# Kernel tuning notes

Measured on AMD Instinct MI355X. Metric: run time of the kernel, lower is better.

## Reference

```python
import jax, jax.numpy as jnp
import numpy as np

EMB_DIM = 1024
ATT_DIM = 1024

def setup_inputs() -> dict:
    key = jax.random.key(0)
    ks = jax.random.split(key, 7)
    B, S = 8, 2048
    x_h = jax.random.normal(ks[0], (B, S, EMB_DIM), dtype=jnp.float32)
    # Linear params (stored as [in, out] for x @ W + b)
    sq = 1.0 / np.sqrt(EMB_DIM)
    Wq = jax.random.uniform(ks[1], (EMB_DIM, ATT_DIM), jnp.float32, -sq, sq)
    bq = jax.random.uniform(ks[2], (ATT_DIM,), jnp.float32, -sq, sq)
    Wk = jax.random.uniform(ks[3], (EMB_DIM, ATT_DIM), jnp.float32, -sq, sq)
    bk = jax.random.uniform(ks[4], (ATT_DIM,), jnp.float32, -sq, sq)
    Wv = jax.random.uniform(ks[5], (EMB_DIM, EMB_DIM), jnp.float32, -sq, sq)
    bv = jax.random.uniform(ks[6], (EMB_DIM,), jnp.float32, -sq, sq)
    return {"x_h": x_h, "Wq": Wq, "bq": bq, "Wk": Wk, "bk": bk, "Wv": Wv, "bv": bv}

def reference(x_h, Wq, bq, Wk, bk, Wv, bv):
    q = x_h @ Wq + bq               # [B,S,att_dim]
    k = x_h @ Wk + bk               # [B,S,att_dim]
    v = x_h @ Wv + bv               # [B,S,emb_dim]
    scale = 1.0 / jnp.sqrt(jnp.asarray(k.shape[-1], q.dtype))
    scores = jnp.einsum('bqd,bkd->bqk', q, k) * scale   # [B,S,S]
    # NOTE: original softmaxes over dim=1 (the QUERY axis), not the key axis.
    attn = jax.nn.softmax(scores, axis=1)
    return jnp.einsum('bqk,bkd->bqd', attn, v)
```

## Files before the change

### kernel.cpp

```cpp
#include <hip/hip_runtime.h>
#include <math.h>

typedef __bf16 bf16x8 __attribute__((ext_vector_type(8)));
typedef float f32x4 __attribute__((ext_vector_type(4)));
typedef unsigned short ushort8 __attribute__((ext_vector_type(8)));
typedef unsigned short ushort4v __attribute__((ext_vector_type(4)));
typedef unsigned short u16;

#define DEVINL __device__ __forceinline__

DEVINL u16 f2bf(float f) {
    union { float f; unsigned u; } a; a.f = f;
    unsigned u = a.u;
    return (u16)((u + 0x7FFFu + ((u >> 16) & 1u)) >> 16);
}
DEVINL float bf2f(u16 h) { return __uint_as_float(((unsigned)h) << 16); }

DEVINL void gload_lds16(const void* g, void* l) {
    __builtin_amdgcn_global_load_lds(
        (__attribute__((address_space(1))) void*)(g),
        (__attribute__((address_space(3))) void*)(l),
        16, 0, 0);
}

template<int EPI>
__global__ __launch_bounds__(512, 2)
void gemm256(const u16* __restrict__ A, int lda, long sAz,
             const u16* __restrict__ B, int ldb, long sBz,
             void* __restrict__ Cv, int ldc, long sCz,
             const float* __restrict__ bias, float* __restrict__ part,
             float scale, int K)
{
    __shared__ u16 lds[65536];
    const int tid = threadIdx.x;
    const int tile_x = blockIdx.x, tile_y = blockIdx.y;
    const long bz = blockIdx.z;

    const u16* Ab = A + bz * sAz;
    const u16* Bb = B + bz * sBz;
    const int row0 = tile_x * 256, col0 = tile_y * 256;

    const int sr = tid >> 2;
    const int csw = ((tid & 3) * 16) ^ (((sr >> 1) & 3) << 4);
    const u16* Ag = Ab + (long)(row0 + sr) * lda + (csw >> 1);
    const u16* Bg = Bb + (long)(col0 + sr) * ldb + (csw >> 1);
    const int dst0 = tid * 8;

    const int lane = tid & 63, wid = tid >> 6;
    const int wm = wid >> 2, wn = wid & 3;
    const int lane_r = lane & 15;
    const int rdcol = (((lane >> 4) * 16) ^ (((lane_r >> 1) & 3) << 4)) >> 1;
    const int arow0 = wm * 128 + lane_r;
    const int brow0 = wn * 64 + lane_r;

    const int NT = K >> 6;
    f32x4 acc[8][4] = {};
    bf16x8 aF0[4], bF0[4], aF1[4], bF1[4];

    auto issueA = [&](int t1, int s, int b) {
        const u16* g = Ag + (long)t1 * 64 + s * 32;
        u16* d = &lds[(b * 2 + s) * 8192 + dst0];
        gload_lds16(g, d);
        gload_lds16(g + (long)128 * lda, d + 4096);
    };
    auto issueB = [&](int t1, int s, int b) {
        const u16* g = Bg + (long)t1 * 64 + s * 32;
        u16* d = &lds[32768 + (b * 2 + s) * 8192 + dst0];
        gload_lds16(g, d);
        gload_lds16(g + (long)128 * ldb, d + 4096);
    };

#define READ_AB(bufv, s, h, SET)                                            \
    _Pragma("unroll")                                                       \
    for (int m = 0; m < 4; ++m)                                             \
        aF##SET[m] = *(const bf16x8*)&lds[((bufv) * 2 + (s)) * 8192 +       \
                         (arow0 + (h) * 64 + m * 16) * 32 + rdcol];         \
    _Pragma("unroll")                                                       \
    for (int n = 0; n < 4; ++n)                                             \
        bF##SET[n] = *(const bf16x8*)&lds[32768 + ((bufv) * 2 + (s)) * 8192 \
                         + (brow0 + n * 16) * 32 + rdcol];

#define MFMA16S(SET, h)                                                     \
    __builtin_amdgcn_s_setprio(1);                                          \
    _Pragma("unroll")                                                       \
    for (int m = 0; m < 4; ++m)                                             \
        _Pragma("unroll")                                                   \
        for (int n = 0; n < 4; ++n)                                         \
            acc[(h) * 4 + m][n] = __builtin_amdgcn_mfma_f32_16x16x32_bf16(  \
                bF##SET[n], aF##SET[m], acc[(h) * 4 + m][n], 0, 0, 0);      \
    __builtin_amdgcn_s_setprio(0);

#define GATE(n)                                                             \
    asm volatile("s_waitcnt vmcnt(" #n ")" ::: "memory");                   \
    __builtin_amdgcn_s_barrier();

    issueA(0, 0, 0); issueB(0, 0, 0);
    issueA(0, 1, 0); issueB(0, 1, 0);
    GATE(4);
    READ_AB(0, 0, 0, 0);

    for (int t = 0; t < NT - 1; ++t) {
        const int buf = t & 1, nbuf = buf ^ 1;
        issueA(t + 1, 0, nbuf); issueB(t + 1, 0, nbuf);
        READ_AB(buf, 0, 1, 1);
        MFMA16S(0, 0);
        GATE(4);
        READ_AB(buf, 1, 0, 0);
        MFMA16S(1, 1);
        issueA(t + 1, 1, nbuf); issueB(t + 1, 1, nbuf);
        READ_AB(buf, 1, 1, 1);
        MFMA16S(0, 0);
        GATE(4);
        READ_AB(nbuf, 0, 0, 0);
        MFMA16S(1, 1);
    }
    {
        const int buf = (NT - 1) & 1;
        READ_AB(buf, 0, 1, 1);
        MFMA16S(0, 0);
        GATE(0);
        READ_AB(buf, 1, 0, 0);
        MFMA16S(1, 1);
        READ_AB(buf, 1, 1, 1);
        MFMA16S(0, 0);
        MFMA16S(1, 1);
    }
#undef READ_AB
#undef MFMA16S
#undef GATE

    const int erow = lane & 15, ecol0 = (lane >> 4) * 4;
    float4 bias4[4];
    if constexpr (EPI == 0) {
#pragma unroll
        for (int nf = 0; nf < 4; ++nf)
            bias4[nf] = *(const float4*)&bias[col0 + wn * 64 + nf * 16 + ecol0];
    }
    f32x4 csum[4] = {};
#pragma unroll
    for (int mf = 0; mf < 8; ++mf) {
        const int gr = row0 + wm * 128 + mf * 16 + erow;
#pragma unroll
        for (int nf = 0; nf < 4; ++nf) {
            const int gc = col0 + wn * 64 + nf * 16 + ecol0;
            f32x4 v = acc[mf][nf];
            if constexpr (EPI == 0) {
                v[0] += bias4[nf].x; v[1] += bias4[nf].y;
                v[2] += bias4[nf].z; v[3] += bias4[nf].w;
                ushort4v o = { f2bf(v[0]), f2bf(v[1]), f2bf(v[2]), f2bf(v[3]) };
                *(ushort4v*)((u16*)Cv + bz * sCz + (long)gr * ldc + gc) = o;
            } else if constexpr (EPI == 1) {
                f32x4 e;
#pragma unroll
                for (int r = 0; r < 4; ++r) e[r] = __expf(v[r] * scale);
                csum[nf] += e;
                ushort4v o = { f2bf(e[0]), f2bf(e[1]), f2bf(e[2]), f2bf(e[3]) };
                *(ushort4v*)((u16*)Cv + bz * sCz + (long)gr * ldc + gc) = o;
            } else {
                *(float4*)((float*)Cv + bz * sCz + (long)gr * ldc + gc) =
                    make_float4(v[0], v[1], v[2], v[3]);
            }
        }
    }
    if constexpr (EPI == 1) {
#pragma unroll
        for (int nf = 0; nf < 4; ++nf)
#pragma unroll
            for (int r = 0; r < 4; ++r) {
                float s = csum[nf][r];
                s += __shfl_xor(s, 1);
                s += __shfl_xor(s, 2);
                s += __shfl_xor(s, 4);
                s += __shfl_xor(s, 8);
                csum[nf][r] = s;
            }
        if ((lane & 15) == 0) {
#pragma unroll
            for (int nf = 0; nf < 4; ++nf) {
                float* p = part + ((bz * 16 + (long)tile_x * 2 + wm) * 2048)
                         + col0 + wn * 64 + nf * 16 + ecol0;
                *(float4*)p = make_float4(csum[nf][0], csum[nf][1],
                                          csum[nf][2], csum[nf][3]);
            }
        }
    }
}

__global__ void cast_x_k(const float* __restrict__ x, u16* __restrict__ o)
{
    const int i = blockIdx.x * 256 + threadIdx.x;
    const float4* xv = (const float4*)x;
    const float4 a = xv[(long)i * 2], b = xv[(long)i * 2 + 1];
    ushort8 r;
    r[0] = f2bf(a.x); r[1] = f2bf(a.y); r[2] = f2bf(a.z); r[3] = f2bf(a.w);
    r[4] = f2bf(b.x); r[5] = f2bf(b.y); r[6] = f2bf(b.z); r[7] = f2bf(b.w);
    *(ushort8*)(o + (long)i * 8) = r;
}

__global__ void wt_k(const float* __restrict__ Wq, const float* __restrict__ Wk,
                     const float* __restrict__ Wv, u16* __restrict__ Wt)
{
    __shared__ float t[32][33];
    const int z = blockIdx.z;
    const float* W = (z == 0) ? Wq : ((z == 1) ? Wk : Wv);
    const int k0 = blockIdx.x * 32, n0 = blockIdx.y * 32;
    const int tx = threadIdx.x, ty = threadIdx.y;
#pragma unroll
    for (int j = 0; j < 32; j += 8)
        t[ty + j][tx] = W[(long)(k0 + ty + j) * 1024 + n0 + tx];
    __syncthreads();
#pragma unroll
    for (int j = 0; j < 32; j += 8)
        Wt[((long)z * 1024 + n0 + ty + j) * 1024 + k0 + tx] = f2bf(t[tx][ty + j]);
}

__global__ void bias_k(const float* __restrict__ bq, const float* __restrict__ bk,
                       const float* __restrict__ bv, float* __restrict__ bcat)
{
    const int i = blockIdx.x * 256 + threadIdx.x;
    bcat[i] = (i < 1024) ? bq[i] : ((i < 2048) ? bk[i - 1024] : bv[i - 2048]);
}

__global__ void rcp_k(const float* __restrict__ part, float* __restrict__ rden)
{
    const int b = blockIdx.y;
    const int k = blockIdx.x * 256 + threadIdx.x;
    float s = 0.f;
#pragma unroll
    for (int c = 0; c < 16; ++c) s += part[((long)b * 16 + c) * 2048 + k];
    rden[b * 2048 + k] = 1.0f / s;
}

__global__ void vt_k(const u16* __restrict__ qkv, const float* __restrict__ rden,
                     u16* __restrict__ Vt)
{
    __shared__ float t[32][33];
    const int b = blockIdx.z;
    const int k0 = blockIdx.x * 32, d0 = blockIdx.y * 32;
    const int tx = threadIdx.x, ty = threadIdx.y;
#pragma unroll
    for (int j = 0; j < 32; j += 8) {
        const int k = k0 + ty + j;
        t[ty + j][tx] = bf2f(qkv[((long)b * 2048 + k) * 3072 + 2048 + d0 + tx])
                        * rden[b * 2048 + k];
    }
    __syncthreads();
#pragma unroll
    for (int j = 0; j < 32; j += 8)
        Vt[((long)b * 1024 + d0 + ty + j) * 2048 + k0 + tx] = f2bf(t[tx][ty + j]);
}

extern "C" void kernel_launch(void* const* d_in, const int* in_sizes, int n_in,
                              void* d_out, int out_size, void* d_ws, size_t ws_size,
                              hipStream_t stream)
{
    const float* x  = (const float*)d_in[0];
    const float* Wq = (const float*)d_in[1];
    const float* bq = (const float*)d_in[2];
    const float* Wk = (const float*)d_in[3];
    const float* bk = (const float*)d_in[4];
    const float* Wv = (const float*)d_in[5];
    const float* bv = (const float*)d_in[6];

    char* ws = (char*)d_ws;
    u16*   qkv  = (u16*)(ws);
    u16*   E    = (u16*)(ws + 100663296);
    u16*   Vt   = (u16*)(ws + 167772160);
    u16*   xb   = (u16*)(ws + 201326592);
    u16*   Wt   = (u16*)(ws + 234881024);
    float* bcat = (float*)(ws + 241172480);
    float* part = (float*)(ws + 241184768);
    float* rden = (float*)(ws + 243281920);

    const long sQKV = (long)2048 * 3072;
    const long sE   = (long)2048 * 2048;
    const long sVt  = (long)1024 * 2048;
    const long sO   = (long)2048 * 1024;

    cast_x_k<<<8192, 256, 0, stream>>>(x, xb);
    wt_k<<<dim3(32, 32, 3), dim3(32, 8), 0, stream>>>(Wq, Wk, Wv, Wt);
    bias_k<<<12, 256, 0, stream>>>(bq, bk, bv, bcat);
    gemm256<0><<<dim3(64, 12, 1), 512, 0, stream>>>(
        xb, 1024, 0, Wt, 1024, 0, qkv, 3072, 0, bcat, nullptr, 0.f, 1024);
    gemm256<1><<<dim3(8, 8, 8), 512, 0, stream>>>(
        qkv, 3072, sQKV, qkv + 1024, 3072, sQKV, E, 2048, sE,
        nullptr, part, 0.03125f, 1024);
    rcp_k<<<dim3(8, 8), 256, 0, stream>>>(part, rden);
    vt_k<<<dim3(64, 32, 8), dim3(32, 8), 0, stream>>>(qkv, rden, Vt);
    gemm256<2><<<dim3(8, 4, 8), 512, 0, stream>>>(
        E, 2048, sE, Vt, 2048, sVt, d_out, 1024, sO,
        nullptr, nullptr, 1.f, 2048);
}
```

Baseline: 301.0 us.

## Switch GEMM inner loop to 32x32x16 MFMA with barrier-fenced ping-pong schedule

Replaces the 16x16x32 bf16 MFMA tiling with 32x32x16 MFMA, so each wave holds a 4x2 grid of 32x32 accumulators and reads fewer, larger fragments from LDS. The main loop is restructured into eight-MFMA phases fenced by s_barrier, interleaving LDS reads and global-to-LDS issues between them. The epilogue is rewritten for the 32x32 output layout, including a wider shuffle reduction for column sums. The goal is to cut LDS read traffic per FLOP and improve MFMA issue density, at the cost of many extra barriers that may serialize waves.

```diff
diff --git a/kernel.cpp b/kernel.cpp
--- a/kernel.cpp
+++ b/kernel.cpp
@@ -3,6 +3,7 @@
 
 typedef __bf16 bf16x8 __attribute__((ext_vector_type(8)));
 typedef float f32x4 __attribute__((ext_vector_type(4)));
+typedef float f32x16 __attribute__((ext_vector_type(16)));
 typedef unsigned short ushort8 __attribute__((ext_vector_type(8)));
 typedef unsigned short ushort4v __attribute__((ext_vector_type(4)));
 typedef unsigned short u16;
@@ -48,14 +49,14 @@
 
     const int lane = tid & 63, wid = tid >> 6;
     const int wm = wid >> 2, wn = wid & 3;
-    const int lane_r = lane & 15;
-    const int rdcol = (((lane >> 4) * 16) ^ (((lane_r >> 1) & 3) << 4)) >> 1;
-    const int arow0 = wm * 128 + lane_r;
-    const int brow0 = wn * 64 + lane_r;
+    const int l31 = lane & 31, eh = lane >> 5;
+    const int eh16 = eh * 16;
+    const int am0 = wm * 128 + l31;
+    const int bn0 = wn * 64 + l31;
 
     const int NT = K >> 6;
-    f32x4 acc[8][4] = {};
-    bf16x8 aF0[4], bF0[4], aF1[4], bF1[4];
+    f32x16 acc[4][2] = {};
+    bf16x8 afr[2][2], bfr[2][2];
 
     auto issueA = [&](int t1, int s, int b) {
         const u16* g = Ag + (long)t1 * 64 + s * 32;
@@ -70,24 +71,37 @@
         gload_lds16(g + (long)128 * ldb, d + 4096);
     };
 
-#define READ_AB(bufv, s, h, SET)                                            \
+#define RDIDX(r, ks) \
+    ((((r) * 64 + ((((ks) * 32) + eh16) ^ ((((r) >> 1) & 3) << 4))) >> 1))
+
+#define READ_A32(bufv, s, h)                                                \
     _Pragma("unroll")                                                       \
-    for (int m = 0; m < 4; ++m)                                             \
-        aF##SET[m] = *(const bf16x8*)&lds[((bufv) * 2 + (s)) * 8192 +       \
-                         (arow0 + (h) * 64 + m * 16) * 32 + rdcol];         \
+    for (int m2 = 0; m2 < 2; ++m2)                                          \
+        _Pragma("unroll")                                                   \
+        for (int ks = 0; ks < 2; ++ks)                                      \
+            afr[m2][ks] = *(const bf16x8*)&lds[((bufv) * 2 + (s)) * 8192    \
+                + RDIDX(am0 + ((h) * 2 + m2) * 32, ks)];
+
+#define READ_B32(bufv, s)                                                   \
     _Pragma("unroll")                                                       \
-    for (int n = 0; n < 4; ++n)                                             \
-        bF##SET[n] = *(const bf16x8*)&lds[32768 + ((bufv) * 2 + (s)) * 8192 \
-                         + (brow0 + n * 16) * 32 + rdcol];
-
-#define MFMA16S(SET, h)                                                     \
+    for (int nf = 0; nf < 2; ++nf)                                          \
+        _Pragma("unroll")                                                   \
+        for (int ks = 0; ks < 2; ++ks)                                      \
+            bfr[nf][ks] = *(const bf16x8*)&lds[32768 +                      \
+                ((bufv) * 2 + (s)) * 8192 + RDIDX(bn0 + nf * 32, ks)];
+
+#define MFMA8(h)                                                            \
     __builtin_amdgcn_s_setprio(1);                                          \
     _Pragma("unroll")                                                       \
-    for (int m = 0; m < 4; ++m)                                             \
+    for (int m2 = 0; m2 < 2; ++m2)                                          \
         _Pragma("unroll")                                                   \
-        for (int n = 0; n < 4; ++n)                                         \
-            acc[(h) * 4 + m][n] = __builtin_amdgcn_mfma_f32_16x16x32_bf16(  \
-                bF##SET[n], aF##SET[m], acc[(h) * 4 + m][n], 0, 0, 0);      \
+        for (int nf = 0; nf < 2; ++nf)                                      \
+            _Pragma("unroll")                                               \
+            for (int ks = 0; ks < 2; ++ks)                                  \
+                acc[(h) * 2 + m2][nf] =                                     \
+                    __builtin_amdgcn_mfma_f32_32x32x16_bf16(                \
+                        bfr[nf][ks], afr[m2][ks], acc[(h) * 2 + m2][nf],    \
+                        0, 0, 0);                                           \
     __builtin_amdgcn_s_setprio(0);
 
 #define GATE(n)                                                             \
@@ -97,91 +111,123 @@
     issueA(0, 0, 0); issueB(0, 0, 0);
     issueA(0, 1, 0); issueB(0, 1, 0);
     GATE(4);
-    READ_AB(0, 0, 0, 0);
 
     for (int t = 0; t < NT - 1; ++t) {
         const int buf = t & 1, nbuf = buf ^ 1;
-        issueA(t + 1, 0, nbuf); issueB(t + 1, 0, nbuf);
-        READ_AB(buf, 0, 1, 1);
-        MFMA16S(0, 0);
-        GATE(4);
-        READ_AB(buf, 1, 0, 0);
-        MFMA16S(1, 1);
-        issueA(t + 1, 1, nbuf); issueB(t + 1, 1, nbuf);
-        READ_AB(buf, 1, 1, 1);
-        MFMA16S(0, 0);
-        GATE(4);
-        READ_AB(nbuf, 0, 0, 0);
-        MFMA16S(1, 1);
+        READ_B32(buf, 0); READ_A32(buf, 0, 0);
+        issueA(t + 1, 0, nbuf);
+        __builtin_amdgcn_s_barrier();
+        MFMA8(0);
+        __builtin_amdgcn_s_barrier();
+        READ_A32(buf, 0, 1);
+        issueB(t + 1, 0, nbuf);
+        asm volatile("s_waitcnt vmcnt(4)" ::: "memory");
+        __builtin_amdgcn_s_barrier();
+        MFMA8(1);
+        __builtin_amdgcn_s_barrier();
+        READ_B32(buf, 1); READ_A32(buf, 1, 0);
+        issueA(t + 1, 1, nbuf);
+        __builtin_amdgcn_s_barrier();
+        MFMA8(0);
+        __builtin_amdgcn_s_barrier();
+        READ_A32(buf, 1, 1);
+        issueB(t + 1, 1, nbuf);
+        asm volatile("s_waitcnt vmcnt(4)" ::: "memory");
+        __builtin_amdgcn_s_barrier();
+        MFMA8(1);
+        __builtin_amdgcn_s_barrier();
     }
     {
         const int buf = (NT - 1) & 1;
-        READ_AB(buf, 0, 1, 1);
-        MFMA16S(0, 0);
-        GATE(0);
-        READ_AB(buf, 1, 0, 0);
-        MFMA16S(1, 1);
-        READ_AB(buf, 1, 1, 1);
-        MFMA16S(0, 0);
-        MFMA16S(1, 1);
-    }
-#undef READ_AB
-#undef MFMA16S
+        READ_B32(buf, 0); READ_A32(buf, 0, 0);
+        __builtin_amdgcn_s_barrier();
+        MFMA8(0);
+        __builtin_amdgcn_s_barrier();
+        READ_A32(buf, 0, 1);
+        asm volatile("s_waitcnt vmcnt(0)" ::: "memory");
+        __builtin_amdgcn_s_barrier();
+        MFMA8(1);
+        __builtin_amdgcn_s_barrier();
+        READ_B32(buf, 1); READ_A32(buf, 1, 0);
+        __builtin_amdgcn_s_barrier();
+        MFMA8(0);
+        __builtin_amdgcn_s_barrier();
+        READ_A32(buf, 1, 1);
+        __builtin_amdgcn_s_barrier();
+        MFMA8(1);
+    }
+#undef READ_A32
+#undef READ_B32
+#undef MFMA8
 #undef GATE
-
-    const int erow = lane & 15, ecol0 = (lane >> 4) * 4;
-    float4 bias4[4];
+#undef RDIDX
+
+    float4 bias4[2][4];
     if constexpr (EPI == 0) {
 #pragma unroll
-        for (int nf = 0; nf < 4; ++nf)
-            bias4[nf] = *(const float4*)&bias[col0 + wn * 64 + nf * 16 + ecol0];
-    }
-    f32x4 csum[4] = {};
-#pragma unroll
-    for (int mf = 0; mf < 8; ++mf) {
-        const int gr = row0 + wm * 128 + mf * 16 + erow;
-#pragma unroll
-        for (int nf = 0; nf < 4; ++nf) {
-            const int gc = col0 + wn * 64 + nf * 16 + ecol0;
-            f32x4 v = acc[mf][nf];
-            if constexpr (EPI == 0) {
-                v[0] += bias4[nf].x; v[1] += bias4[nf].y;
-                v[2] += bias4[nf].z; v[3] += bias4[nf].w;
-                ushort4v o = { f2bf(v[0]), f2bf(v[1]), f2bf(v[2]), f2bf(v[3]) };
-                *(ushort4v*)((u16*)Cv + bz * sCz + (long)gr * ldc + gc) = o;
-            } else if constexpr (EPI == 1) {
-                f32x4 e;
-#pragma unroll
-                for (int r = 0; r < 4; ++r) e[r] = __expf(v[r] * scale);
-                csum[nf] += e;
-                ushort4v o = { f2bf(e[0]), f2bf(e[1]), f2bf(e[2]), f2bf(e[3]) };
-                *(ushort4v*)((u16*)Cv + bz * sCz + (long)gr * ldc + gc) = o;
-            } else {
-                *(float4*)((float*)Cv + bz * sCz + (long)gr * ldc + gc) =
-                    make_float4(v[0], v[1], v[2], v[3]);
+        for (int nf = 0; nf < 2; ++nf)
+#pragma unroll
+            for (int rg = 0; rg < 4; ++rg)
+                bias4[nf][rg] = *(const float4*)
+                    &bias[col0 + wn * 64 + nf * 32 + rg * 8 + eh * 4];
+    }
+    f32x4 csum[2][4] = {};
+#pragma unroll
+    for (int mf = 0; mf < 4; ++mf) {
+        const int gr = row0 + wm * 128 + mf * 32 + l31;
+#pragma unroll
+        for (int nf = 0; nf < 2; ++nf) {
+#pragma unroll
+            for (int rg = 0; rg < 4; ++rg) {
+                const int gc = col0 + wn * 64 + nf * 32 + rg * 8 + eh * 4;
+                float v0 = acc[mf][nf][rg * 4 + 0];
+                float v1 = acc[mf][nf][rg * 4 + 1];
+                float v2 = acc[mf][nf][rg * 4 + 2];
+                float v3 = acc[mf][nf][rg * 4 + 3];
+                if constexpr (EPI == 0) {
+                    v0 += bias4[nf][rg].x; v1 += bias4[nf][rg].y;
+                    v2 += bias4[nf][rg].z; v3 += bias4[nf][rg].w;
+                    ushort4v o = { f2bf(v0), f2bf(v1), f2bf(v2), f2bf(v3) };
+                    *(ushort4v*)((u16*)Cv + bz * sCz + (long)gr * ldc + gc) = o;
+                } else if constexpr (EPI == 1) {
+                    v0 = __expf(v0 * scale); v1 = __expf(v1 * scale);
+                    v2 = __expf(v2 * scale); v3 = __expf(v3 * scale);
+                    csum[nf][rg][0] += v0; csum[nf][rg][1] += v1;
+                    csum[nf][rg][2] += v2; csum[nf][rg][3] += v3;
+                    ushort4v o = { f2bf(v0), f2bf(v1), f2bf(v2), f2bf(v3) };
+                    *(ushort4v*)((u16*)Cv + bz * sCz + (long)gr * ldc + gc) = o;
+                } else {
+                    *(float4*)((float*)Cv + bz * sCz + (long)gr * ldc + gc) =
+                        make_float4(v0, v1, v2, v3);
+                }
             }
         }
     }
     if constexpr (EPI == 1) {
 #pragma unroll
-        for (int nf = 0; nf < 4; ++nf)
-#pragma unroll
-            for (int r = 0; r < 4; ++r) {
-                float s = csum[nf][r];
-                s += __shfl_xor(s, 1);
-                s += __shfl_xor(s, 2);
-                s += __shfl_xor(s, 4);
-                s += __shfl_xor(s, 8);
-                csum[nf][r] = s;
-            }
-        if ((lane & 15) == 0) {
-#pragma unroll
-            for (int nf = 0; nf < 4; ++nf) {
-                float* p = part + ((bz * 16 + (long)tile_x * 2 + wm) * 2048)
-                         + col0 + wn * 64 + nf * 16 + ecol0;
-                *(float4*)p = make_float4(csum[nf][0], csum[nf][1],
-                                          csum[nf][2], csum[nf][3]);
-            }
+        for (int nf = 0; nf < 2; ++nf)
+#pragma unroll
+            for (int rg = 0; rg < 4; ++rg)
+#pragma unroll
+                for (int r = 0; r < 4; ++r) {
+                    float s = csum[nf][rg][r];
+                    s += __shfl_xor(s, 1);
+                    s += __shfl_xor(s, 2);
+                    s += __shfl_xor(s, 4);
+                    s += __shfl_xor(s, 8);
+                    s += __shfl_xor(s, 16);
+                    csum[nf][rg][r] = s;
+                }
+        if (l31 == 0) {
+#pragma unroll
+            for (int nf = 0; nf < 2; ++nf)
+#pragma unroll
+                for (int rg = 0; rg < 4; ++rg) {
+                    float* p = part + ((bz * 16 + (long)tile_x * 2 + wm) * 2048)
+                             + col0 + wn * 64 + nf * 32 + rg * 8 + eh * 4;
+                    *(float4*)p = make_float4(csum[nf][rg][0], csum[nf][rg][1],
+                                              csum[nf][rg][2], csum[nf][rg][3]);
+                }
         }
     }
 }
```

Measured after the change: 344.1 us. 1.14x slower.

## Replace double-buffered K-loop with 4-slot ring buffer prefetching three stages ahead

Applied to the files above, without the earlier changes.

Restructures the GEMM main loop from a double-buffered 64-wide K tile with interleaved half-tile register sets into a 4-slot ring of 32-wide K stages, issuing loads three stages ahead. Each phase loads all 8 A and 4 B fragments, then issues 32 MFMAs, with one vmcnt wait and barrier per stage. The deeper prefetch is meant to hide global-to-LDS latency better, at the cost of more barriers per K, more live fragment registers, and less interleaving of LDS reads with MFMAs.

```diff
diff --git a/kernel.cpp b/kernel.cpp
--- a/kernel.cpp
+++ b/kernel.cpp
@@ -53,81 +53,58 @@
     const int arow0 = wm * 128 + lane_r;
     const int brow0 = wn * 64 + lane_r;
 
-    const int NT = K >> 6;
+    const int NP = K >> 5;
     f32x4 acc[8][4] = {};
-    bf16x8 aF0[4], bF0[4], aF1[4], bF1[4];
-
-    auto issueA = [&](int t1, int s, int b) {
-        const u16* g = Ag + (long)t1 * 64 + s * 32;
-        u16* d = &lds[(b * 2 + s) * 8192 + dst0];
-        gload_lds16(g, d);
-        gload_lds16(g + (long)128 * lda, d + 4096);
+
+    auto issuePair = [&](int j2) {
+        const int r = (j2 & 3) * 8192;
+        const u16* ga = Ag + (long)j2 * 32;
+        const u16* gb = Bg + (long)j2 * 32;
+        gload_lds16(ga,                      &lds[r + dst0]);
+        gload_lds16(ga + (long)128 * lda,    &lds[r + 4096 + dst0]);
+        gload_lds16(gb,                      &lds[32768 + r + dst0]);
+        gload_lds16(gb + (long)128 * ldb,    &lds[32768 + r + 4096 + dst0]);
     };
-    auto issueB = [&](int t1, int s, int b) {
-        const u16* g = Bg + (long)t1 * 64 + s * 32;
-        u16* d = &lds[32768 + (b * 2 + s) * 8192 + dst0];
-        gload_lds16(g, d);
-        gload_lds16(g + (long)128 * ldb, d + 4096);
-    };
-
-#define READ_AB(bufv, s, h, SET)                                            \
-    _Pragma("unroll")                                                       \
-    for (int m = 0; m < 4; ++m)                                             \
-        aF##SET[m] = *(const bf16x8*)&lds[((bufv) * 2 + (s)) * 8192 +       \
-                         (arow0 + (h) * 64 + m * 16) * 32 + rdcol];         \
-    _Pragma("unroll")                                                       \
-    for (int n = 0; n < 4; ++n)                                             \
-        bF##SET[n] = *(const bf16x8*)&lds[32768 + ((bufv) * 2 + (s)) * 8192 \
-                         + (brow0 + n * 16) * 32 + rdcol];
-
-#define MFMA16S(SET, h)                                                     \
-    __builtin_amdgcn_s_setprio(1);                                          \
-    _Pragma("unroll")                                                       \
-    for (int m = 0; m < 4; ++m)                                             \
+
+#define PHASE_BODY(JV)                                                      \
+    {                                                                       \
+        const int r = ((JV) & 3) * 8192;                                    \
+        bf16x8 bfr[4], af[8];                                               \
         _Pragma("unroll")                                                   \
         for (int n = 0; n < 4; ++n)                                         \
-            acc[(h) * 4 + m][n] = __builtin_amdgcn_mfma_f32_16x16x32_bf16(  \
-                bF##SET[n], aF##SET[m], acc[(h) * 4 + m][n], 0, 0, 0);      \
-    __builtin_amdgcn_s_setprio(0);
-
-#define GATE(n)                                                             \
-    asm volatile("s_waitcnt vmcnt(" #n ")" ::: "memory");                   \
+            bfr[n] = *(const bf16x8*)&lds[32768 + r +                       \
+                         (brow0 + n * 16) * 32 + rdcol];                    \
+        _Pragma("unroll")                                                   \
+        for (int m = 0; m < 8; ++m)                                         \
+            af[m] = *(const bf16x8*)&lds[r + (arow0 + m * 16) * 32 + rdcol];\
+        __builtin_amdgcn_s_setprio(1);                                      \
+        _Pragma("unroll")                                                   \
+        for (int m = 0; m < 8; ++m)                                         \
+            _Pragma("unroll")                                               \
+            for (int n = 0; n < 4; ++n)                                     \
+                acc[m][n] = __builtin_amdgcn_mfma_f32_16x16x32_bf16(        \
+                    bfr[n], af[m], acc[m][n], 0, 0, 0);                     \
+        __builtin_amdgcn_s_setprio(0);                                      \
+    }
+
+    issuePair(0); issuePair(1); issuePair(2);
+    asm volatile("s_waitcnt vmcnt(8)" ::: "memory");
     __builtin_amdgcn_s_barrier();
 
-    issueA(0, 0, 0); issueB(0, 0, 0);
-    issueA(0, 1, 0); issueB(0, 1, 0);
-    GATE(4);
-    READ_AB(0, 0, 0, 0);
-
-    for (int t = 0; t < NT - 1; ++t) {
-        const int buf = t & 1, nbuf = buf ^ 1;
-        issueA(t + 1, 0, nbuf); issueB(t + 1, 0, nbuf);
-        READ_AB(buf, 0, 1, 1);
-        MFMA16S(0, 0);
-        GATE(4);
-        READ_AB(buf, 1, 0, 0);
-        MFMA16S(1, 1);
-        issueA(t + 1, 1, nbuf); issueB(t + 1, 1, nbuf);
-        READ_AB(buf, 1, 1, 1);
-        MFMA16S(0, 0);
-        GATE(4);
-        READ_AB(nbuf, 0, 0, 0);
-        MFMA16S(1, 1);
-    }
-    {
-        const int buf = (NT - 1) & 1;
-        READ_AB(buf, 0, 1, 1);
-        MFMA16S(0, 0);
-        GATE(0);
-        READ_AB(buf, 1, 0, 0);
-        MFMA16S(1, 1);
-        READ_AB(buf, 1, 1, 1);
-        MFMA16S(0, 0);
-        MFMA16S(1, 1);
-    }
-#undef READ_AB
-#undef MFMA16S
-#undef GATE
+    for (int j = 0; j < NP - 3; ++j) {
+        issuePair(j + 3);
+        PHASE_BODY(j);
+        asm volatile("s_waitcnt vmcnt(8)" ::: "memory");
+        __builtin_amdgcn_s_barrier();
+    }
+    PHASE_BODY(NP - 3);
+    asm volatile("s_waitcnt vmcnt(4)" ::: "memory");
+    __builtin_amdgcn_s_barrier();
+    PHASE_BODY(NP - 2);
+    asm volatile("s_waitcnt vmcnt(0)" ::: "memory");
+    __builtin_amdgcn_s_barrier();
+    PHASE_BODY(NP - 1);
+#undef PHASE_BODY
 
     const int erow = lane & 15, ecol0 = (lane >> 4) * 4;
     float4 bias4[4];
```

Measured after the change: 307.8 us. +2.3%, slower.
